# Optimization experiments

Hardware: AMD Instinct MI355X
Metric: run time of the kernel (lower is better)

## Reference

```python
import jax, jax.numpy as jnp
import numpy as np

NUM_EMB = 100000
EMB = 64
NUM_CTNS = 10
HEADS = 4
ATT = 32
HD = HEADS * ATT  # 128
FIELDS = 32       # 20 onehot + 2 multihot + 10 ctns
B = 8192


def _linear_params(key, out_f, in_f):
    kw, kb = jax.random.split(key)
    W = jax.random.normal(kw, (out_f, in_f), jnp.float32) * 0.05
    b = jax.random.normal(kb, (out_f,), jnp.float32) * 0.05
    return W, b


def setup_inputs() -> dict:
    key = jax.random.key(0)
    ks = jax.random.split(key, 16)
    inp = {
        'onehot_i': jax.random.randint(ks[0], (B, 20), 0, NUM_EMB),
        'onehot_x': jax.random.uniform(ks[1], (B, 20), jnp.float32),
        'mh_i': jax.random.randint(ks[2], (2, B, 50), 0, NUM_EMB),
        'mh_x': jax.random.uniform(ks[3], (2, B, 50), jnp.float32),
        'ctns': jax.random.normal(ks[4], (B, NUM_CTNS), jnp.float32),
        'xx': jax.random.normal(ks[5], (NUM_EMB, EMB), jnp.float32),
        'xy': jax.random.normal(ks[6], (NUM_CTNS, EMB), jnp.float32),
    }
    # layer 1 attention params (emb -> h*d)
    names1 = ['QW1', 'Qb1', 'KW1', 'Kb1', 'VW1', 'Vb1', 'RW1', 'Rb1']
    for i in range(4):
        W, b = _linear_params(ks[7 + i], HD, EMB)
        inp[names1[2 * i]] = W
        inp[names1[2 * i + 1]] = b
    # layer 2 attention params (h*d -> h*d)
    names2 = ['QW2', 'Qb2', 'KW2', 'Kb2', 'VW2', 'Vb2', 'RW2', 'Rb2']
    for i in range(4):
        W, b = _linear_params(ks[11 + i], HD, HD)
        inp[names2[2 * i]] = W
        inp[names2[2 * i + 1]] = b
    lW, lb = _linear_params(ks[15], 1, FIELDS * HD)
    inp['logitW'] = lW
    inp['logitb'] = lb
    return inp


def _attn_block(y, QW, Qb, KW, Kb, VW, Vb, RW, Rb):
    # y: [B, F, D]; heads are head-major in the h*d output dim (matches torch split/cat)
    b, f, _ = y.shape
    Q = (y @ QW.T + Qb).reshape(b, f, HEADS, ATT)
    K = (y @ KW.T + Kb).reshape(b, f, HEADS, ATT)
    V = (y @ VW.T + Vb).reshape(b, f, HEADS, ATT)
    Res = y @ RW.T + Rb
    scores = jnp.einsum('bqhd,bkhd->bhqk', Q, K)  # unscaled, as in source
    A = jax.nn.softmax(scores, axis=-1)
    O = jnp.einsum('bhqk,bkhd->bqhd', A, V).reshape(b, f, HD)
    return jax.nn.relu(O + Res)


def reference(onehot_i, onehot_x, mh_i, mh_x, ctns, xx, xy,
              QW1, Qb1, KW1, Kb1, VW1, Vb1, RW1, Rb1,
              QW2, Qb2, KW2, Kb2, VW2, Vb2, RW2, Rb2,
              logitW, logitb):
    onehot_fields = xx[onehot_i] * onehot_x[..., None]                 # [B,20,EMB]
    mh_fields = (xx[mh_i] * mh_x[..., None]).sum(axis=2)               # [2,B,EMB]
    mh_fields = jnp.transpose(mh_fields, (1, 0, 2))                    # [B,2,EMB]
    ctns_fields = ctns[..., None] * xy                                 # [B,10,EMB]
    y = jnp.concatenate([onehot_fields, mh_fields, ctns_fields], axis=1)  # [B,32,EMB]
    y = _attn_block(y, QW1, Qb1, KW1, Kb1, VW1, Vb1, RW1, Rb1)
    y = _attn_block(y, QW2, Qb2, KW2, Kb2, VW2, Vb2, RW2, Rb2)
    flat = y.reshape(y.shape[0], -1)                                   # [B, 32*128]
    out = jax.nn.sigmoid(flat @ logitW.T + logitb)
    return out.squeeze()
```

## Files before the change

### kernel.cpp

```cpp
#include <hip/hip_runtime.h>
#include <hip/hip_bf16.h>


#define NSAMP 8192
#define S_Y1 72
#define S_T 36

typedef __attribute__((ext_vector_type(8))) short bf8_t;
typedef __attribute__((ext_vector_type(16))) float f16v;

__device__ __forceinline__ short f2bf(float f) {
  unsigned u = __float_as_uint(f);
  u += 0x7fffu + ((u >> 16) & 1u);
  return (short)(u >> 16);
}
__device__ __forceinline__ unsigned pack2(float a, float b) {
  __hip_bfloat162 h = __float22bfloat162_rn(float2{a, b});
  union { __hip_bfloat162 h2; unsigned u; } cvt;
  cvt.h2 = h;
  return cvt.u;
}
__device__ __forceinline__ float bf2f(short s) {
  return __uint_as_float(((unsigned)(unsigned short)s) << 16);
}
__device__ __forceinline__ float rcp_fast(float x) {
  return __builtin_amdgcn_rcpf(x);
}
__device__ __forceinline__ f16v mfma32(bf8_t a, bf8_t b, f16v c) {
  return __builtin_amdgcn_mfma_f32_32x32x16_bf16(a, b, c, 0, 0, 0);
}

template<int KS, bool HAS_NEXT>
__device__ __forceinline__ void projPF(const bf8_t (&af)[2][KS],
                                       const short* __restrict__ W,
                                       const float* __restrict__ bias,
                                       int fragBase,
                                       const short* __restrict__ Wnext,
                                       int fbNext, int n0, int col,
                                       bf8_t (&pre)[4], f16v (&o)[2]) {
  constexpr int PF = (KS < 4) ? KS : 4;
  bf8_t nxt[4];
  if constexpr (HAS_NEXT) {
#pragma unroll
    for (int i = 0; i < 4; ++i)
      nxt[i] = *(const bf8_t*)&Wnext[fbNext + i * 512];
  }
  float bb = bias[n0 + col];
#pragma unroll
  for (int i = 0; i < 16; ++i) { o[0][i] = bb; o[1][i] = bb; }
#pragma unroll
  for (int kc = 0; kc < KS; ++kc) {
    bf8_t w;
    if (kc < PF) w = pre[kc];
    else w = *(const bf8_t*)&W[fragBase + kc * 512];
    o[0] = mfma32(af[0][kc], w, o[0]);
    o[1] = mfma32(af[1][kc], w, o[1]);
  }
  if constexpr (HAS_NEXT) {
#pragma unroll
    for (int i = 0; i < 4; ++i) pre[i] = nxt[i];
  }
}

__device__ __forceinline__ void storeQuad(short* tile, int stride, int g, int h2,
                                          int col, float a0, float a1, float a2,
                                          float a3) {
  unsigned p01 = pack2(a0, a1);
  unsigned p23 = pack2(a2, a3);
  int rb = 8 * g + 4 * h2;
  tile[(rb + 0) * stride + col] = (short)(p01 & 0xffffu);
  tile[(rb + 1) * stride + col] = (short)(p01 >> 16);
  tile[(rb + 2) * stride + col] = (short)(p23 & 0xffffu);
  tile[(rb + 3) * stride + col] = (short)(p23 >> 16);
}

template<int D_IN, bool FUSE>
__device__ void attn_layer(const short* yIn0, const short* yIn1,
                           short* yOut0, short* yOut1,
                           const short* __restrict__ Wq, const short* __restrict__ Wk,
                           const short* __restrict__ Wv, const short* __restrict__ Wr,
                           const float* __restrict__ bq, const float* __restrict__ bk,
                           const float* __restrict__ bvp, const float* __restrict__ br,
                           short* bQ0, short* bK0, short* bQ1, short* bK1,
                           const short* __restrict__ lwF,
                           const short* __restrict__ WnlQ, int fbNext,
                           int n0, int col, int h2, bf8_t (&pre)[4],
                           float (&pp)[2]) {
  constexpr int KS = D_IN / 16;
  const short* yIn[2] = {yIn0, yIn1};
  short* bQ[2] = {bQ0, bQ1};
  short* bK[2] = {bK0, bK1};
  const int head = n0 >> 5;
  const int lane = h2 * 32 + col;
  const int fragBase = head * KS * 512 + lane * 8;

  bf8_t af[2][KS];
#pragma unroll
  for (int sp = 0; sp < 2; ++sp)
#pragma unroll
    for (int kc = 0; kc < KS; ++kc) {
      if constexpr (FUSE) {
        int gsw = (kc * 2 + h2) ^ (col & 15);
        af[sp][kc] = *(const bf8_t*)&yIn[sp][col * 128 + (gsw << 3)];
      } else {
        af[sp][kc] = *(const bf8_t*)&yIn[sp][col * S_Y1 + kc * 16 + h2 * 8];
      }
    }
  if constexpr (!FUSE)
    __syncthreads();

  f16v acc[2];

  projPF<KS, true>(af, Wq, bq, fragBase, Wk, fragBase, n0, col, pre, acc);
#pragma unroll
  for (int sp = 0; sp < 2; ++sp)
#pragma unroll
    for (int g = 0; g < 4; ++g)
      storeQuad(bQ[sp], S_T, g, h2, col, acc[sp][4 * g + 0], acc[sp][4 * g + 1],
                acc[sp][4 * g + 2], acc[sp][4 * g + 3]);

  projPF<KS, true>(af, Wk, bk, fragBase, Wr, fragBase, n0, col, pre, acc);
#pragma unroll
  for (int sp = 0; sp < 2; ++sp)
#pragma unroll
    for (int g = 0; g < 4; ++g)
      storeQuad(bK[sp], S_T, g, h2, col, acc[sp][4 * g + 0], acc[sp][4 * g + 1],
                acc[sp][4 * g + 2], acc[sp][4 * g + 3]);

  f16v res[2];
  projPF<KS, true>(af, Wr, br, fragBase, Wv, fragBase, n0, col, pre, res);

#pragma unroll
  for (int sp = 0; sp < 2; ++sp) {
    f16v z;
#pragma unroll
    for (int i = 0; i < 16; ++i) z[i] = 0.f;
#pragma unroll
    for (int kc = 0; kc < 2; ++kc) {
      bf8_t qa = *(const bf8_t*)&bQ[sp][col * S_T + kc * 16 + h2 * 8];
      bf8_t kb = *(const bf8_t*)&bK[sp][col * S_T + kc * 16 + h2 * 8];
      z = mfma32(qa, kb, z);
    }
#pragma unroll
    for (int g = 0; g < 4; ++g)
      storeQuad(bQ[sp], S_T, g, h2, col,
                __expf(z[4 * g + 0]), __expf(z[4 * g + 1]),
                __expf(z[4 * g + 2]), __expf(z[4 * g + 3]));
  }

  projPF<KS, !FUSE>(af, Wv, bvp, fragBase, WnlQ, fbNext, n0, col, pre, acc);
#pragma unroll
  for (int sp = 0; sp < 2; ++sp)
#pragma unroll
    for (int g = 0; g < 4; ++g) {
      uint2 pk;
      pk.x = pack2(acc[sp][g * 4 + 0], acc[sp][g * 4 + 1]);
      pk.y = pack2(acc[sp][g * 4 + 2], acc[sp][g * 4 + 3]);
      *(uint2*)&bK[sp][col * S_T + 8 * g + 4 * h2] = pk;
    }

  short4 l4b[4];
  if constexpr (FUSE) {
#pragma unroll
    for (int g = 0; g < 4; ++g)
      l4b[g] = *(const short4*)&lwF[(head * 4 + g) * 256 + lane * 4];
  }

  const short onebf = (short)0x3F80;
  bf8_t ones = {onebf, onebf, onebf, onebf, onebf, onebf, onebf, onebf};
  f16v pv[2], sums[2];
#pragma unroll
  for (int sp = 0; sp < 2; ++sp) {
#pragma unroll
    for (int i = 0; i < 16; ++i) { pv[sp][i] = 0.f; sums[sp][i] = 0.f; }
#pragma unroll
    for (int kc = 0; kc < 2; ++kc) {
      bf8_t pa = *(const bf8_t*)&bQ[sp][col * S_T + kc * 16 + h2 * 8];
      bf8_t vb = *(const bf8_t*)&bK[sp][col * S_T + kc * 16 + h2 * 8];
      pv[sp] = mfma32(pa, vb, pv[sp]);
      sums[sp] = mfma32(pa, ones, sums[sp]);
    }
  }

  if constexpr (FUSE) {
#pragma unroll
    for (int g = 0; g < 4; ++g) {
      short4 l4 = l4b[g];
#pragma unroll
      for (int r = 0; r < 4; ++r) {
        int reg = g * 4 + r;
        float lw = bf2f((r == 0) ? l4.x : (r == 1) ? l4.y : (r == 2) ? l4.z : l4.w);
        pp[0] += fmaxf(fmaf(pv[0][reg], rcp_fast(sums[0][reg]), res[0][reg]), 0.f) * lw;
        pp[1] += fmaxf(fmaf(pv[1][reg], rcp_fast(sums[1][reg]), res[1][reg]), 0.f) * lw;
      }
    }
  } else {
    short* yOut[2] = {yOut0, yOut1};
    const int cg = head * 4 + (col >> 3);
    const int cw = col & 7;
#pragma unroll
    for (int sp = 0; sp < 2; ++sp)
#pragma unroll
      for (int g = 0; g < 4; ++g) {
        float v[4];
#pragma unroll
        for (int r = 0; r < 4; ++r)
          v[r] = fmaxf(fmaf(pv[sp][4 * g + r], rcp_fast(sums[sp][4 * g + r]),
                            res[sp][4 * g + r]), 0.f);
        unsigned p01 = pack2(v[0], v[1]);
        unsigned p23 = pack2(v[2], v[3]);
        int rb = 8 * g + 4 * h2;
        short s4[4] = {(short)(p01 & 0xffffu), (short)(p01 >> 16),
                       (short)(p23 & 0xffffu), (short)(p23 >> 16)};
#pragma unroll
        for (int r = 0; r < 4; ++r) {
          int row = rb + r;
          yOut[sp][row * 128 + ((cg ^ (row & 15)) << 3) + cw] = s4[r];
        }
      }
  }
}

__global__ __launch_bounds__(256, 3) void autoint_main(
    const int* __restrict__ onehot_i, const float* __restrict__ onehot_x,
    const int* __restrict__ mh_i, const float* __restrict__ mh_x,
    const float* __restrict__ ctns, const float* __restrict__ xx,
    const float* __restrict__ xy,
    const float* __restrict__ bq1, const float* __restrict__ bk1,
    const float* __restrict__ bv1, const float* __restrict__ br1,
    const float* __restrict__ bq2, const float* __restrict__ bk2,
    const float* __restrict__ bv2, const float* __restrict__ br2,
    const float* __restrict__ logitb, const short* __restrict__ wbf,
    float* __restrict__ out) {
  __shared__ __align__(16) short scr[2][9216];
  __shared__ __align__(16) short y2s[2][4096];

  const int t = threadIdx.x;
  const int head = t >> 6;
  const int lane = t & 63;
  const int col = lane & 31;
  const int h2 = lane >> 5;
  const int n0 = head * 32;
  const int s0 = blockIdx.x * 2;

  short* bQ0 = &scr[0][(head * 2 + 0) * 1152];
  short* bK0 = &scr[0][(head * 2 + 1) * 1152];
  short* bQ1 = &scr[1][(head * 2 + 0) * 1152];
  short* bK1 = &scr[1][(head * 2 + 1) * 1152];

  const int fb1 = head * 4 * 512 + lane * 8;
  const int fb2 = head * 8 * 512 + lane * 8;
  bf8_t pre[4];
#pragma unroll
  for (int i = 0; i < 4; ++i) pre[i] = *(const bf8_t*)&wbf[fb1 + i * 512];

  int*   mhi_s = (int*)  &scr[0][2304];
  float* mhx_s = (float*)&scr[0][2704];

  const int e4 = t & 15, f0 = t >> 4;

  int oh_r[2][2]; float oh_w[2][2];
#pragma unroll
  for (int se = 0; se < 2; ++se) {
    oh_r[0][se] = onehot_i[(s0 + se) * 20 + f0];
    oh_w[0][se] = onehot_x[(s0 + se) * 20 + f0];
  }
  if (t < 64) {
#pragma unroll
    for (int se = 0; se < 2; ++se) {
      oh_r[1][se] = onehot_i[(s0 + se) * 20 + 16 + f0];
      oh_w[1][se] = onehot_x[(s0 + se) * 20 + 16 + f0];
    }
  }
  if (t < 160) {
    int ci = t >> 4;
    float4 xv = *(const float4*)&xy[ci * 64 + e4 * 4];
    float cv0 = ctns[(s0 + 0) * 10 + ci];
    float cv1 = ctns[(s0 + 1) * 10 + ci];
    uint2 w0; w0.x = pack2(cv0 * xv.x, cv0 * xv.y); w0.y = pack2(cv0 * xv.z, cv0 * xv.w);
    *(uint2*)&scr[0][(22 + ci) * S_Y1 + e4 * 4] = w0;
    uint2 w1; w1.x = pack2(cv1 * xv.x, cv1 * xv.y); w1.y = pack2(cv1 * xv.z, cv1 * xv.w);
    *(uint2*)&scr[1][(22 + ci) * S_Y1 + e4 * 4] = w1;
  }
  if (t < 200) {
    int g = t / 50, k = t - g * 50;
    int se = g >> 1, j = g & 1;
    mhi_s[(se * 2 + j) * 50 + k] = mh_i[(j * NSAMP + s0 + se) * 50 + k];
    mhx_s[(se * 2 + j) * 50 + k] = mh_x[(j * NSAMP + s0 + se) * 50 + k];
  }
  __syncthreads();

  float4 g0[2], g1[2];
#pragma unroll
  for (int se = 0; se < 2; ++se)
    g0[se] = *(const float4*)&xx[oh_r[0][se] * 64 + e4 * 4];
  if (t < 64) {
#pragma unroll
    for (int se = 0; se < 2; ++se)
      g1[se] = *(const float4*)&xx[oh_r[1][se] * 64 + e4 * 4];
  }

  {
    const int slot = t >> 3, ks = t & 7;
    const int j = slot >> 4, e4m = slot & 15;
#pragma unroll
    for (int se = 0; se < 2; ++se) {
      const int base = (se * 2 + j) * 50;
      float4 xv[7]; float wt[7];
#pragma unroll
      for (int i = 0; i < 7; ++i) {
        int k = ks + 8 * i;
        int ok = (k < 50);
        int row = ok ? mhi_s[base + k] : 0;
        wt[i] = ok ? mhx_s[base + k] : 0.f;
        xv[i] = *(const float4*)&xx[row * 64 + e4m * 4];
      }
      float a0 = 0.f, a1 = 0.f, a2 = 0.f, a3 = 0.f;
#pragma unroll
      for (int i = 0; i < 7; ++i) {
        a0 += xv[i].x * wt[i]; a1 += xv[i].y * wt[i];
        a2 += xv[i].z * wt[i]; a3 += xv[i].w * wt[i];
      }
#pragma unroll
      for (int d = 1; d < 8; d <<= 1) {
        a0 += __shfl_xor(a0, d); a1 += __shfl_xor(a1, d);
        a2 += __shfl_xor(a2, d); a3 += __shfl_xor(a3, d);
      }
      if (ks == 0) {
        uint2 w; w.x = pack2(a0, a1); w.y = pack2(a2, a3);
        *(uint2*)&scr[se][(20 + j) * S_Y1 + e4m * 4] = w;
      }
    }
  }

#pragma unroll
  for (int se = 0; se < 2; ++se) {
    float xw = oh_w[0][se];
    uint2 w; w.x = pack2(g0[se].x * xw, g0[se].y * xw);
    w.y = pack2(g0[se].z * xw, g0[se].w * xw);
    *(uint2*)&scr[se][f0 * S_Y1 + e4 * 4] = w;
  }
  if (t < 64) {
#pragma unroll
    for (int se = 0; se < 2; ++se) {
      float xw = oh_w[1][se];
      uint2 w; w.x = pack2(g1[se].x * xw, g1[se].y * xw);
      w.y = pack2(g1[se].z * xw, g1[se].w * xw);
      *(uint2*)&scr[se][(16 + f0) * S_Y1 + e4 * 4] = w;
    }
  }
  __syncthreads();

  float pp[2] = {0.f, 0.f};
  attn_layer<64, false>(&scr[0][0], &scr[1][0], &y2s[0][0], &y2s[1][0],
      wbf + 0, wbf + 8192, wbf + 16384, wbf + 24576,
      bq1, bk1, bv1, br1, bQ0, bK0, bQ1, bK1, nullptr,
      wbf + 32768, fb2, n0, col, h2, pre, pp);
  __syncthreads();
  attn_layer<128, true>(&y2s[0][0], &y2s[1][0], nullptr, nullptr,
      wbf + 32768, wbf + 49152, wbf + 65536, wbf + 81920,
      bq2, bk2, bv2, br2, bQ0, bK0, bQ1, bK1, wbf + 98304,
      wbf, 0, n0, col, h2, pre, pp);

  float* red0 = (float*)bQ0;
  float* red1 = (float*)bQ1;
#pragma unroll
  for (int off = 32; off > 0; off >>= 1) {
    pp[0] += __shfl_xor(pp[0], off);
    pp[1] += __shfl_xor(pp[1], off);
  }
  if (lane == 0) { red0[0] = pp[0]; red1[0] = pp[1]; }
  __syncthreads();
  if (t < 2) {
    const short* base = t == 0 ? &scr[0][0] : &scr[1][0];
    float zz = logitb[0];
#pragma unroll
    for (int h = 0; h < 4; ++h)
      zz += *(const float*)&base[(h * 2) * 1152];
    out[s0 + t] = 1.f / (1.f + __expf(-zz));
  }
}

__global__ void convert_w(const float* __restrict__ qw1, const float* __restrict__ kw1,
                          const float* __restrict__ vw1, const float* __restrict__ rw1,
                          const float* __restrict__ qw2, const float* __restrict__ kw2,
                          const float* __restrict__ vw2, const float* __restrict__ rw2,
                          const float* __restrict__ lw, short* __restrict__ outw) {
  int i = blockIdx.x * 256 + threadIdx.x;
  if (i >= 102400) return;
  float v;
  if (i < 32768) {
    int tsel = i >> 13, d = i & 8191;
    int e = d & 7, lane = (d >> 3) & 63, kc = (d >> 9) & 3, h = (d >> 11) & 3;
    int col = lane & 31, h2 = lane >> 5;
    int j = (h * 32 + col) * 64 + kc * 16 + h2 * 8 + e;
    const float* src = tsel == 0 ? qw1 : tsel == 1 ? kw1 : tsel == 2 ? vw1 : rw1;
    v = src[j];
  } else if (i < 98304) {
    int k = i - 32768;
    int tsel = k >> 14, d = k & 16383;
    int e = d & 7, lane = (d >> 3) & 63, kc = (d >> 9) & 7, h = (d >> 12) & 3;
    int col = lane & 31, h2 = lane >> 5;
    int j = (h * 32 + col) * 128 + kc * 16 + h2 * 8 + e;
    const float* src = tsel == 0 ? qw2 : tsel == 1 ? kw2 : tsel == 2 ? vw2 : rw2;
    v = src[j];
  } else {
    int d = i - 98304;
    int r = d & 3, lane = (d >> 2) & 63, g = (d >> 8) & 3, h = (d >> 10) & 3;
    int col = lane & 31, h2 = lane >> 5;
    v = lw[(8 * g + 4 * h2 + r) * 128 + h * 32 + col];
  }
  outw[i] = f2bf(v);
}

extern "C" void kernel_launch(void* const* d_in, const int* in_sizes, int n_in,
                              void* d_out, int out_size, void* d_ws, size_t ws_size,
                              hipStream_t stream) {
  short* wbf = (short*)d_ws;
  convert_w<<<400, 256, 0, stream>>>(
      (const float*)d_in[7], (const float*)d_in[9], (const float*)d_in[11],
      (const float*)d_in[13], (const float*)d_in[15], (const float*)d_in[17],
      (const float*)d_in[19], (const float*)d_in[21], (const float*)d_in[23], wbf);
  autoint_main<<<NSAMP / 2, 256, 0, stream>>>(
      (const int*)d_in[0], (const float*)d_in[1], (const int*)d_in[2],
      (const float*)d_in[3], (const float*)d_in[4], (const float*)d_in[5],
      (const float*)d_in[6],
      (const float*)d_in[8], (const float*)d_in[10], (const float*)d_in[12],
      (const float*)d_in[14], (const float*)d_in[16], (const float*)d_in[18],
      (const float*)d_in[20], (const float*)d_in[22], (const float*)d_in[24],
      wbf, (float*)d_out);
}
```

Before: 242.6 us.

## Build layer-1 MFMA operands directly in registers from gathered embeddings

```diff
diff --git a/kernel.cpp b/kernel.cpp
--- a/kernel.cpp
+++ b/kernel.cpp
@@ -3,7 +3,6 @@
 
 
 #define NSAMP 8192
-#define S_Y1 72
 #define S_T 36
 
 typedef __attribute__((ext_vector_type(8))) short bf8_t;
@@ -28,6 +27,14 @@
 }
 __device__ __forceinline__ f16v mfma32(bf8_t a, bf8_t b, f16v c) {
   return __builtin_amdgcn_mfma_f32_32x32x16_bf16(a, b, c, 0, 0, 0);
+}
+__device__ __forceinline__ bf8_t pack8s(float4 a, float4 b, float w) {
+  union { bf8_t v; unsigned u[4]; } r;
+  r.u[0] = pack2(a.x * w, a.y * w);
+  r.u[1] = pack2(a.z * w, a.w * w);
+  r.u[2] = pack2(b.x * w, b.y * w);
+  r.u[3] = pack2(b.z * w, b.w * w);
+  return r.v;
 }
 
 template<int KS, bool HAS_NEXT>
@@ -75,7 +82,7 @@
 }
 
 template<int D_IN, bool FUSE>
-__device__ void attn_layer(const short* yIn0, const short* yIn1,
+__device__ void attn_layer(const bf8_t (&af)[2][D_IN / 16],
                            short* yOut0, short* yOut1,
                            const short* __restrict__ Wq, const short* __restrict__ Wk,
                            const short* __restrict__ Wv, const short* __restrict__ Wr,
@@ -87,25 +94,12 @@
                            int n0, int col, int h2, bf8_t (&pre)[4],
                            float (&pp)[2]) {
   constexpr int KS = D_IN / 16;
-  const short* yIn[2] = {yIn0, yIn1};
   short* bQ[2] = {bQ0, bQ1};
   short* bK[2] = {bK0, bK1};
   const int head = n0 >> 5;
   const int lane = h2 * 32 + col;
   const int fragBase = head * KS * 512 + lane * 8;
 
-  bf8_t af[2][KS];
-#pragma unroll
-  for (int sp = 0; sp < 2; ++sp)
-#pragma unroll
-    for (int kc = 0; kc < KS; ++kc) {
-      if constexpr (FUSE) {
-        int gsw = (kc * 2 + h2) ^ (col & 15);
-        af[sp][kc] = *(const bf8_t*)&yIn[sp][col * 128 + (gsw << 3)];
-      } else {
-        af[sp][kc] = *(const bf8_t*)&yIn[sp][col * S_Y1 + kc * 16 + h2 * 8];
-      }
-    }
   if constexpr (!FUSE)
     __syncthreads();
 
@@ -254,50 +248,36 @@
 #pragma unroll
   for (int i = 0; i < 4; ++i) pre[i] = *(const bf8_t*)&wbf[fb1 + i * 512];
 
-  int*   mhi_s = (int*)  &scr[0][2304];
-  float* mhx_s = (float*)&scr[0][2704];
-
-  const int e4 = t & 15, f0 = t >> 4;
-
-  int oh_r[2][2]; float oh_w[2][2];
-#pragma unroll
-  for (int se = 0; se < 2; ++se) {
-    oh_r[0][se] = onehot_i[(s0 + se) * 20 + f0];
-    oh_w[0][se] = onehot_x[(s0 + se) * 20 + f0];
-  }
-  if (t < 64) {
+  bf8_t af1[2][4];
+  if (col < 20) {
 #pragma unroll
     for (int se = 0; se < 2; ++se) {
-      oh_r[1][se] = onehot_i[(s0 + se) * 20 + 16 + f0];
-      oh_w[1][se] = onehot_x[(s0 + se) * 20 + 16 + f0];
-    }
-  }
-  if (t < 160) {
-    int ci = t >> 4;
-    float4 xv = *(const float4*)&xy[ci * 64 + e4 * 4];
-    float cv0 = ctns[(s0 + 0) * 10 + ci];
-    float cv1 = ctns[(s0 + 1) * 10 + ci];
-    uint2 w0; w0.x = pack2(cv0 * xv.x, cv0 * xv.y); w0.y = pack2(cv0 * xv.z, cv0 * xv.w);
-    *(uint2*)&scr[0][(22 + ci) * S_Y1 + e4 * 4] = w0;
-    uint2 w1; w1.x = pack2(cv1 * xv.x, cv1 * xv.y); w1.y = pack2(cv1 * xv.z, cv1 * xv.w);
-    *(uint2*)&scr[1][(22 + ci) * S_Y1 + e4 * 4] = w1;
-  }
-  if (t < 200) {
-    int g = t / 50, k = t - g * 50;
-    int se = g >> 1, j = g & 1;
-    mhi_s[(se * 2 + j) * 50 + k] = mh_i[(j * NSAMP + s0 + se) * 50 + k];
-    mhx_s[(se * 2 + j) * 50 + k] = mh_x[(j * NSAMP + s0 + se) * 50 + k];
-  }
-  __syncthreads();
-
-  float4 g0[2], g1[2];
-#pragma unroll
-  for (int se = 0; se < 2; ++se)
-    g0[se] = *(const float4*)&xx[oh_r[0][se] * 64 + e4 * 4];
-  if (t < 64) {
-#pragma unroll
-    for (int se = 0; se < 2; ++se)
-      g1[se] = *(const float4*)&xx[oh_r[1][se] * 64 + e4 * 4];
+      int r = onehot_i[(s0 + se) * 20 + col];
+      float w = onehot_x[(s0 + se) * 20 + col];
+      const float* rp = &xx[r * 64 + h2 * 8];
+#pragma unroll
+      for (int kc = 0; kc < 4; ++kc) {
+        float4 a = *(const float4*)&rp[kc * 16];
+        float4 b = *(const float4*)&rp[kc * 16 + 4];
+        af1[se][kc] = pack8s(a, b, w);
+      }
+    }
+  } else if (col >= 22) {
+    const int ci = col - 22;
+    const float* rp = &xy[ci * 64 + h2 * 8];
+    float4 xa[4], xb[4];
+#pragma unroll
+    for (int kc = 0; kc < 4; ++kc) {
+      xa[kc] = *(const float4*)&rp[kc * 16];
+      xb[kc] = *(const float4*)&rp[kc * 16 + 4];
+    }
+#pragma unroll
+    for (int se = 0; se < 2; ++se) {
+      float cv = ctns[(s0 + se) * 10 + ci];
+#pragma unroll
+      for (int kc = 0; kc < 4; ++kc)
+        af1[se][kc] = pack8s(xa[kc], xb[kc], cv);
+    }
   }
 
   {
@@ -305,16 +285,21 @@
     const int j = slot >> 4, e4m = slot & 15;
 #pragma unroll
     for (int se = 0; se < 2; ++se) {
-      const int base = (se * 2 + j) * 50;
-      float4 xv[7]; float wt[7];
+      const int sg = s0 + se;
+      const int* ip = &mh_i[(j * NSAMP + sg) * 50];
+      const float* xp = &mh_x[(j * NSAMP + sg) * 50];
+      int rw[7]; float wt[7];
 #pragma unroll
       for (int i = 0; i < 7; ++i) {
         int k = ks + 8 * i;
         int ok = (k < 50);
-        int row = ok ? mhi_s[base + k] : 0;
-        wt[i] = ok ? mhx_s[base + k] : 0.f;
-        xv[i] = *(const float4*)&xx[row * 64 + e4m * 4];
-      }
+        rw[i] = ok ? ip[k] : 0;
+        wt[i] = ok ? xp[k] : 0.f;
+      }
+      float4 xv[7];
+#pragma unroll
+      for (int i = 0; i < 7; ++i)
+        xv[i] = *(const float4*)&xx[rw[i] * 64 + e4m * 4];
       float a0 = 0.f, a1 = 0.f, a2 = 0.f, a3 = 0.f;
 #pragma unroll
       for (int i = 0; i < 7; ++i) {
@@ -328,36 +313,37 @@
       }
       if (ks == 0) {
         uint2 w; w.x = pack2(a0, a1); w.y = pack2(a2, a3);
-        *(uint2*)&scr[se][(20 + j) * S_Y1 + e4m * 4] = w;
-      }
-    }
-  }
-
-#pragma unroll
-  for (int se = 0; se < 2; ++se) {
-    float xw = oh_w[0][se];
-    uint2 w; w.x = pack2(g0[se].x * xw, g0[se].y * xw);
-    w.y = pack2(g0[se].z * xw, g0[se].w * xw);
-    *(uint2*)&scr[se][f0 * S_Y1 + e4 * 4] = w;
-  }
-  if (t < 64) {
-#pragma unroll
-    for (int se = 0; se < 2; ++se) {
-      float xw = oh_w[1][se];
-      uint2 w; w.x = pack2(g1[se].x * xw, g1[se].y * xw);
-      w.y = pack2(g1[se].z * xw, g1[se].w * xw);
-      *(uint2*)&scr[se][(16 + f0) * S_Y1 + e4 * 4] = w;
+        *(uint2*)&scr[se][j * 64 + e4m * 4] = w;
+      }
     }
   }
   __syncthreads();
 
+  if (col == 20 || col == 21) {
+    const int j = col - 20;
+#pragma unroll
+    for (int se = 0; se < 2; ++se)
+#pragma unroll
+      for (int kc = 0; kc < 4; ++kc)
+        af1[se][kc] = *(const bf8_t*)&scr[se][j * 64 + kc * 16 + h2 * 8];
+  }
+
   float pp[2] = {0.f, 0.f};
-  attn_layer<64, false>(&scr[0][0], &scr[1][0], &y2s[0][0], &y2s[1][0],
+  attn_layer<64, false>(af1, &y2s[0][0], &y2s[1][0],
       wbf + 0, wbf + 8192, wbf + 16384, wbf + 24576,
       bq1, bk1, bv1, br1, bQ0, bK0, bQ1, bK1, nullptr,
       wbf + 32768, fb2, n0, col, h2, pre, pp);
   __syncthreads();
-  attn_layer<128, true>(&y2s[0][0], &y2s[1][0], nullptr, nullptr,
+
+  bf8_t af2[2][8];
+#pragma unroll
+  for (int sp = 0; sp < 2; ++sp)
+#pragma unroll
+    for (int kc = 0; kc < 8; ++kc) {
+      int gsw = (kc * 2 + h2) ^ (col & 15);
+      af2[sp][kc] = *(const bf8_t*)&y2s[sp][col * 128 + (gsw << 3)];
+    }
+  attn_layer<128, true>(af2, nullptr, nullptr,
       wbf + 32768, wbf + 49152, wbf + 65536, wbf + 81920,
       bq2, bk2, bv2, br2, bQ0, bK0, bQ1, bK1, wbf + 98304,
       wbf, 0, n0, col, h2, pre, pp);
```

New measurement: 258.7 us. 1.07x slower.
